# Kernel tuning notes

Measured on AMD Instinct MI355X. Metric: run time of the kernel, lower is better.

Reference implementation:

```python
import jax, jax.numpy as jnp
import numpy as np

# MANO kinematic tree (21-joint ordering: wrist=0, fingers 1..15, tips 16..20)
PARENTS16 = [0, 0, 1, 2, 0, 4, 5, 0, 7, 8, 0, 10, 11, 0, 13, 14]
MANOIDX = [2, 3, 17, 5, 6, 18, 8, 9, 20, 11, 12, 19, 14, 15, 16]
MANOPDX = [1, 2, 3, 4, 5, 6, 7, 8, 9, 10, 11, 12, 13, 14, 15]
CHILDREN = [[1, 2, 3, 17, 4, 5, 6, 18, 7, 8, 9, 20, 10, 11, 12, 19, 13, 14, 15, 16],
            [2, 3, 17], [3, 17], [17], [5, 6, 18], [6, 18], [18],
            [8, 9, 20], [9, 20], [20], [11, 12, 19], [12, 19], [19],
            [14, 15, 16], [15, 16], [16]]
TIPS = [(17, 3), (18, 6), (20, 9), (19, 12), (16, 15)]
EPS = 1e-8


def _skew(v):
    # v: (N,3) -> (N,3,3) skew-symmetric cross-product matrix
    z = jnp.zeros_like(v[..., 0])
    return jnp.stack([
        jnp.stack([z, -v[..., 2], v[..., 1]], -1),
        jnp.stack([v[..., 2], z, -v[..., 0]], -1),
        jnp.stack([-v[..., 1], v[..., 0], z], -1)], -2)


def _rot_between(v0, v1):
    # Rodrigues rotation taking direction v0 to v1. (N,3),(N,3) -> (N,3,3)
    n0 = v0 / (jnp.linalg.norm(v0, axis=-1, keepdims=True) + EPS)
    n1 = v1 / (jnp.linalg.norm(v1, axis=-1, keepdims=True) + EPS)
    c = jnp.sum(n0 * n1, axis=-1)
    ax = jnp.cross(n0, n1)
    s = jnp.linalg.norm(ax, axis=-1)
    axn = ax / (s[..., None] + EPS)
    K = _skew(axn)
    I = jnp.eye(3, dtype=v0.dtype)
    return I + s[:, None, None] * K + (1.0 - c)[:, None, None] * (K @ K)


def _kabsch(a, b):
    # rotation R (N,3,3) minimizing ||R a_i - b_i|| over joints; a,b: (N,21,3)
    H = jnp.einsum('nji,njk->nik', a, b)
    U, S, Vt = jnp.linalg.svd(H)
    V = jnp.swapaxes(Vt, -1, -2)
    d = jnp.linalg.det(V @ jnp.swapaxes(U, -1, -2))
    scale = jnp.stack([jnp.ones_like(d), jnp.ones_like(d), d], axis=-1)  # (N,3)
    Vd = V * scale[:, None, :]
    return Vd @ jnp.swapaxes(U, -1, -2)


def setup_inputs() -> dict:
    key = jax.random.key(0)
    k1, k2 = jax.random.split(key)
    N = 400000
    joint_gt = jax.random.normal(k1, (N, 21, 3), dtype=jnp.float32)
    tempJ = jax.random.normal(k2, (N, 21, 3), dtype=jnp.float32)
    return {"joint_gt": joint_gt, "tempJ": tempJ}


def _kinematic_match(joint_gt, tempJ):
    oriWrist = joint_gt[:, :1]
    jg = joint_gt - oriWrist                  # GT joints, wrist-centered
    tJ0 = tempJ - tempJ[:, :1]                # template (tempJori), wrist-centered
    tJ = tJ0

    # global wrist rotation aligning template to GT (wristRotTorch)
    Rw = _kabsch(tJ, jg)
    tJ = jnp.einsum('nij,ncj->nci', Rw, tJ)   # apply to all joints (wrist stays 0)

    Grot = [None] * 16
    locals_rot = [None] * 16
    Grot[0] = Rw

    # greedy per-joint rotation fitting with parent->child propagation
    for idx, i in enumerate(MANOIDX):
        pi = MANOPDX[idx]
        v0 = tJ[:, i] - tJ[:, pi]
        v1 = jg[:, i] - tJ[:, pi]
        r = _rot_between(v0, v1)              # (N,3,3)
        t0 = tJ[:, pi]
        ch = CHILDREN[pi]
        rel = tJ[:, ch] - t0[:, None]
        tJ = tJ.at[:, ch].set(jnp.einsum('nij,ncj->nci', r, rel) + t0[:, None])
        p16 = PARENTS16[idx + 1]
        GpR = Grot[p16]
        Grot[idx + 1] = r @ GpR               # transformG = L @ Gp (rotation part)
        # transformLmano = inv(Gp) @ L @ Gp  (rotation part)
        locals_rot[idx + 1] = jnp.einsum('nji,njk,nkl->nil', GpR, r, GpR)

    # rotate2joint: forward kinematics from mano-local rotations over template
    Gfk = [None] * 16
    Gfk[0] = Rw
    pos = jnp.zeros_like(jg)
    for k in range(1, 16):
        p = PARENTS16[k]
        off = tJ0[:, k] - tJ0[:, p]
        pos = pos.at[:, k].set(jnp.einsum('nij,nj->ni', Gfk[p], off) + pos[:, p])
        Gfk[k] = Gfk[p] @ locals_rot[k]
    for tip, par in TIPS:
        off = tJ0[:, tip] - tJ0[:, par]
        pos = pos.at[:, tip].set(jnp.einsum('nij,nj->ni', Gfk[par], off) + pos[:, par])

    return pos + oriWrist


def reference(joint_gt, tempJ):
    return _kinematic_match(joint_gt, tempJ)
```

## Files before the change

### kernel.cpp

```cpp
#include <hip/hip_runtime.h>

#define DEVI __device__ __forceinline__

static constexpr float KEPS = 1e-8f;

DEVI float frcp(float x) { return __builtin_amdgcn_rcpf(x); }
DEVI float frsq(float x) { return __builtin_amdgcn_rsqf(x); }

template<int P, int Q>
DEVI void jrot(float A[4][4], float V[4][4]) {
  float apq = A[P][Q];
  if (fabsf(apq) > 1e-20f) {
    float theta = (A[Q][Q] - A[P][P]) * 0.5f * frcp(apq);
    float t = copysignf(frcp(fabsf(theta) + sqrtf(theta * theta + 1.0f)), theta);
    float c = frsq(t * t + 1.0f);
    float s = t * c;
#pragma unroll
    for (int k = 0; k < 4; ++k) { float u = A[k][P], v = A[k][Q]; A[k][P] = c*u - s*v; A[k][Q] = s*u + c*v; }
#pragma unroll
    for (int k = 0; k < 4; ++k) { float u = A[P][k], v = A[Q][k]; A[P][k] = c*u - s*v; A[Q][k] = s*u + c*v; }
#pragma unroll
    for (int k = 0; k < 4; ++k) { float u = V[k][P], v = V[k][Q]; V[k][P] = c*u - s*v; V[k][Q] = s*u + c*v; }
  }
}

template<int C>
DEVI void rotc(float t[21][3], float px, float py, float pz,
               float r00, float r01, float r02,
               float r10, float r11, float r12,
               float r20, float r21, float r22) {
  float x = t[C][0] - px, y = t[C][1] - py, z = t[C][2] - pz;
  t[C][0] = r00*x + r01*y + r02*z + px;
  t[C][1] = r10*x + r11*y + r12*z + py;
  t[C][2] = r20*x + r21*y + r22*z + pz;
}

template<int PI, int I, int C0, int C1, int C2, int NC>
DEVI void bone(float t[21][3], const float g[21][3]) {
  float px = t[PI][0], py = t[PI][1], pz = t[PI][2];
  float v0x = t[I][0] - px, v0y = t[I][1] - py, v0z = t[I][2] - pz;
  float v1x = g[I][0] - px, v1y = g[I][1] - py, v1z = g[I][2] - pz;
  float in0 = frcp(sqrtf(v0x*v0x + v0y*v0y + v0z*v0z) + KEPS);
  float in1 = frcp(sqrtf(v1x*v1x + v1y*v1y + v1z*v1z) + KEPS);
  float ax = v0x*in0, ay = v0y*in0, az = v0z*in0;
  float bx = v1x*in1, by = v1y*in1, bz = v1z*in1;
  float c = ax*bx + ay*by + az*bz;
  float cx = ay*bz - az*by;
  float cy = az*bx - ax*bz;
  float cz = ax*by - ay*bx;
  float s = sqrtf(cx*cx + cy*cy + cz*cz);
  float is = frcp(s + KEPS);
  float kx = cx*is, ky = cy*is, kz = cz*is;
  float omc = 1.0f - c;
  float r00 = 1.0f - omc*(ky*ky + kz*kz);
  float r11 = 1.0f - omc*(kx*kx + kz*kz);
  float r22 = 1.0f - omc*(kx*kx + ky*ky);
  float kxy = omc*kx*ky, kxz = omc*kx*kz, kyz = omc*ky*kz;
  float skx = s*kx, sky = s*ky, skz = s*kz;
  float r01 = kxy - skz, r10 = kxy + skz;
  float r02 = kxz + sky, r20 = kxz - sky;
  float r12 = kyz - skx, r21 = kyz + skx;
  rotc<C0>(t, px, py, pz, r00, r01, r02, r10, r11, r12, r20, r21, r22);
  if constexpr (NC > 1) rotc<C1>(t, px, py, pz, r00, r01, r02, r10, r11, r12, r20, r21, r22);
  if constexpr (NC > 2) rotc<C2>(t, px, py, pz, r00, r01, r02, r10, r11, r12, r20, r21, r22);
}

template<int B, int T>
DEVI void finger(float t[21][3], const float g[21][3]) {
  bone<B,     B + 1, B + 1, B + 2, T, 3>(t, g);
  bone<B + 1, B + 2, B + 2, T,     T, 2>(t, g);
  bone<B + 2, T,     T,     T,     T, 1>(t, g);
}

DEVI void stage_half(float* lds, const float* __restrict__ src, long long off,
                     long long total, bool fullblk, int tid) {
  if (fullblk) {
    const float4* s4 = (const float4*)(src + off);
#pragma unroll
    for (int it = 0; it < 8; ++it) { int i = it * 64 + tid; if (i < 504) ((float4*)lds)[i] = s4[i]; }
  } else {
    for (int i = tid; i < 2016; i += 64) { long long gi = off + i; lds[i] = (gi < total) ? src[gi] : 0.0f; }
  }
}

__global__ void __launch_bounds__(64)
kin_kernel(const float* __restrict__ joint_gt, const float* __restrict__ tempJ,
           float* __restrict__ out, int N) {
  __shared__ float lds[32 * 63];
  const int tid = threadIdx.x;
  const int half = tid >> 5;
  const int lane = tid & 31;
  const long long base = (long long)blockIdx.x * (64LL * 63);
  const long long total = (long long)N * 63;
  const bool fullblk = (base + 64LL * 63) <= total;

  float t[21][3], g[21][3];
  float wx, wy, wz;

#pragma unroll 1
  for (int h = 0; h < 2; ++h) {
    stage_half(lds, tempJ, base + (long long)h * 2016, total, fullblk, tid);
    __syncthreads();
    if (half == h) {
      const float* p = lds + lane * 63;
      float rx = p[0], ry = p[1], rz = p[2];
#pragma unroll
      for (int j = 0; j < 21; ++j) {
        t[j][0] = p[3 * j + 0] - rx;
        t[j][1] = p[3 * j + 1] - ry;
        t[j][2] = p[3 * j + 2] - rz;
      }
    }
    __syncthreads();
  }

#pragma unroll 1
  for (int h = 0; h < 2; ++h) {
    stage_half(lds, joint_gt, base + (long long)h * 2016, total, fullblk, tid);
    __syncthreads();
    if (half == h) {
      const float* p = lds + lane * 63;
      wx = p[0]; wy = p[1]; wz = p[2];
#pragma unroll
      for (int j = 0; j < 21; ++j) {
        g[j][0] = p[3 * j + 0] - wx;
        g[j][1] = p[3 * j + 1] - wy;
        g[j][2] = p[3 * j + 2] - wz;
      }
    }
    __syncthreads();
  }

  float H[3][3] = {{0, 0, 0}, {0, 0, 0}, {0, 0, 0}};
#pragma unroll
  for (int j = 0; j < 21; ++j)
#pragma unroll
    for (int a = 0; a < 3; ++a)
#pragma unroll
      for (int b = 0; b < 3; ++b)
        H[a][b] += t[j][a] * g[j][b];

  float Sxx = H[0][0], Sxy = H[0][1], Sxz = H[0][2];
  float Syx = H[1][0], Syy = H[1][1], Syz = H[1][2];
  float Szx = H[2][0], Szy = H[2][1], Szz = H[2][2];
  float A[4][4] = {
    {  Sxx + Syy + Szz, Syz - Szy,        Szx - Sxz,        Sxy - Syx },
    {  Syz - Szy,       Sxx - Syy - Szz,  Sxy + Syx,        Szx + Sxz },
    {  Szx - Sxz,       Sxy + Syx,       -Sxx + Syy - Szz,  Syz + Szy },
    {  Sxy - Syx,       Szx + Sxz,        Syz + Szy,       -Sxx - Syy + Szz }};
  float V[4][4] = {{1,0,0,0},{0,1,0,0},{0,0,1,0},{0,0,0,1}};
#pragma unroll 1
  for (int sw = 0; sw < 6; ++sw) {
    jrot<0,1>(A, V); jrot<0,2>(A, V); jrot<0,3>(A, V);
    jrot<1,2>(A, V); jrot<1,3>(A, V); jrot<2,3>(A, V);
  }
  float e  = A[0][0];
  float qw = V[0][0], qx = V[1][0], qy = V[2][0], qz = V[3][0];
#define PICK(K) { bool bb = A[K][K] > e; e = bb ? A[K][K] : e; \
  qw = bb ? V[0][K] : qw; qx = bb ? V[1][K] : qx; qy = bb ? V[2][K] : qy; qz = bb ? V[3][K] : qz; }
  PICK(1) PICK(2) PICK(3)
#undef PICK
  float qn = frsq(qw*qw + qx*qx + qy*qy + qz*qz);
  qw *= qn; qx *= qn; qy *= qn; qz *= qn;
  float R00 = 1.0f - 2.0f*(qy*qy + qz*qz), R01 = 2.0f*(qx*qy - qw*qz), R02 = 2.0f*(qx*qz + qw*qy);
  float R10 = 2.0f*(qx*qy + qw*qz), R11 = 1.0f - 2.0f*(qx*qx + qz*qz), R12 = 2.0f*(qy*qz - qw*qx);
  float R20 = 2.0f*(qx*qz - qw*qy), R21 = 2.0f*(qy*qz + qw*qx), R22 = 1.0f - 2.0f*(qx*qx + qy*qy);

#pragma unroll
  for (int j = 1; j < 21; ++j) {
    float x = t[j][0], y = t[j][1], z = t[j][2];
    t[j][0] = R00*x + R01*y + R02*z;
    t[j][1] = R10*x + R11*y + R12*z;
    t[j][2] = R20*x + R21*y + R22*z;
  }

  finger<1, 17>(t, g);
  finger<4, 18>(t, g);
  finger<7, 20>(t, g);
  finger<10, 19>(t, g);
  finger<13, 16>(t, g);

#pragma unroll 1
  for (int h = 0; h < 2; ++h) {
    if (half == h) {
      float* p = lds + lane * 63;
#pragma unroll
      for (int j = 0; j < 21; ++j) {
        p[3 * j + 0] = t[j][0] + wx;
        p[3 * j + 1] = t[j][1] + wy;
        p[3 * j + 2] = t[j][2] + wz;
      }
    }
    __syncthreads();
    const long long off = base + (long long)h * 2016;
    if (fullblk) {
      float4* d4 = (float4*)(out + off);
#pragma unroll
      for (int it = 0; it < 8; ++it) { int i = it * 64 + tid; if (i < 504) d4[i] = ((const float4*)lds)[i]; }
    } else {
      for (int i = tid; i < 2016; i += 64) { long long gi = off + i; if (gi < total) out[gi] = lds[i]; }
    }
    __syncthreads();
  }
}

extern "C" void kernel_launch(void* const* d_in, const int* in_sizes, int n_in,
                              void* d_out, int out_size, void* d_ws, size_t ws_size,
                              hipStream_t stream) {
  const float* joint_gt = (const float*)d_in[0];
  const float* tempJ    = (const float*)d_in[1];
  float* out = (float*)d_out;
  int N = in_sizes[0] / 63;
  int blocks = (N + 63) / 64;
  hipLaunchKernelGGL(kin_kernel, dim3(blocks), dim3(64), 0, stream,
                     joint_gt, tempJ, out, N);
}
```

Measured before the change: 325.7 us.

## Use per-wave LDS staging without block barriers and pack four waves per block

Each wave now owns its own LDS slice and stages inputs and outputs in four 16-item rounds, so all __syncthreads calls are removed and the code relies on wave-level lockstep. Blocks grow from 64 to 256 threads with launch bounds (256,4), and the LDS per wave shrinks. The aim is to cut barrier stalls and raise occupancy for this register-heavy kernel. In exchange there are more, smaller staging rounds, and correctness depends on implicit wave synchronization through LDS.

```diff
diff --git a/kernel.cpp b/kernel.cpp
--- a/kernel.cpp
+++ b/kernel.cpp
@@ -72,37 +72,33 @@
   bone<B + 2, T,     T,     T,     T, 1>(t, g);
 }
 
-DEVI void stage_half(float* lds, const float* __restrict__ src, long long off,
-                     long long total, bool fullblk, int tid) {
-  if (fullblk) {
-    const float4* s4 = (const float4*)(src + off);
-#pragma unroll
-    for (int it = 0; it < 8; ++it) { int i = it * 64 + tid; if (i < 504) ((float4*)lds)[i] = s4[i]; }
-  } else {
-    for (int i = tid; i < 2016; i += 64) { long long gi = off + i; lds[i] = (gi < total) ? src[gi] : 0.0f; }
-  }
-}
-
-__global__ void __launch_bounds__(64)
+__global__ void __launch_bounds__(256, 4)
 kin_kernel(const float* __restrict__ joint_gt, const float* __restrict__ tempJ,
            float* __restrict__ out, int N) {
-  __shared__ float lds[32 * 63];
-  const int tid = threadIdx.x;
-  const int half = tid >> 5;
-  const int lane = tid & 31;
-  const long long base = (long long)blockIdx.x * (64LL * 63);
+  __shared__ float lds[4][16 * 63];
+  const int wave = threadIdx.x >> 6;
+  const int lane = threadIdx.x & 63;
+  float* buf = &lds[wave][0];
+  const long long item0 = ((long long)blockIdx.x * 4 + wave) * 64;
+  if (item0 >= N) return;
+  const bool wfull = (item0 + 64) <= (long long)N;
   const long long total = (long long)N * 63;
-  const bool fullblk = (base + 64LL * 63) <= total;
 
   float t[21][3], g[21][3];
   float wx, wy, wz;
 
 #pragma unroll 1
-  for (int h = 0; h < 2; ++h) {
-    stage_half(lds, tempJ, base + (long long)h * 2016, total, fullblk, tid);
-    __syncthreads();
-    if (half == h) {
-      const float* p = lds + lane * 63;
+  for (int r = 0; r < 4; ++r) {
+    const long long off = (item0 + r * 16) * 63;
+    if (wfull) {
+      const float4* s4 = (const float4*)(tempJ + off);
+#pragma unroll
+      for (int k = 0; k < 4; ++k) { int i = k * 64 + lane; if (i < 252) ((float4*)buf)[i] = s4[i]; }
+    } else {
+      for (int i = lane; i < 1008; i += 64) { long long gi = off + i; buf[i] = (gi < total) ? tempJ[gi] : 0.0f; }
+    }
+    if ((lane >> 4) == r) {
+      const float* p = buf + (lane & 15) * 63;
       float rx = p[0], ry = p[1], rz = p[2];
 #pragma unroll
       for (int j = 0; j < 21; ++j) {
@@ -111,15 +107,20 @@
         t[j][2] = p[3 * j + 2] - rz;
       }
     }
-    __syncthreads();
-  }
-
-#pragma unroll 1
-  for (int h = 0; h < 2; ++h) {
-    stage_half(lds, joint_gt, base + (long long)h * 2016, total, fullblk, tid);
-    __syncthreads();
-    if (half == h) {
-      const float* p = lds + lane * 63;
+  }
+
+#pragma unroll 1
+  for (int r = 0; r < 4; ++r) {
+    const long long off = (item0 + r * 16) * 63;
+    if (wfull) {
+      const float4* s4 = (const float4*)(joint_gt + off);
+#pragma unroll
+      for (int k = 0; k < 4; ++k) { int i = k * 64 + lane; if (i < 252) ((float4*)buf)[i] = s4[i]; }
+    } else {
+      for (int i = lane; i < 1008; i += 64) { long long gi = off + i; buf[i] = (gi < total) ? joint_gt[gi] : 0.0f; }
+    }
+    if ((lane >> 4) == r) {
+      const float* p = buf + (lane & 15) * 63;
       wx = p[0]; wy = p[1]; wz = p[2];
 #pragma unroll
       for (int j = 0; j < 21; ++j) {
@@ -128,7 +129,6 @@
         g[j][2] = p[3 * j + 2] - wz;
       }
     }
-    __syncthreads();
   }
 
   float H[3][3] = {{0, 0, 0}, {0, 0, 0}, {0, 0, 0}};
@@ -181,9 +181,9 @@
   finger<13, 16>(t, g);
 
 #pragma unroll 1
-  for (int h = 0; h < 2; ++h) {
-    if (half == h) {
-      float* p = lds + lane * 63;
+  for (int r = 0; r < 4; ++r) {
+    if ((lane >> 4) == r) {
+      float* p = buf + (lane & 15) * 63;
 #pragma unroll
       for (int j = 0; j < 21; ++j) {
         p[3 * j + 0] = t[j][0] + wx;
@@ -191,16 +191,14 @@
         p[3 * j + 2] = t[j][2] + wz;
       }
     }
-    __syncthreads();
-    const long long off = base + (long long)h * 2016;
-    if (fullblk) {
+    const long long off = (item0 + r * 16) * 63;
+    if (wfull) {
       float4* d4 = (float4*)(out + off);
 #pragma unroll
-      for (int it = 0; it < 8; ++it) { int i = it * 64 + tid; if (i < 504) d4[i] = ((const float4*)lds)[i]; }
+      for (int k = 0; k < 4; ++k) { int i = k * 64 + lane; if (i < 252) d4[i] = ((const float4*)buf)[i]; }
     } else {
-      for (int i = tid; i < 2016; i += 64) { long long gi = off + i; if (gi < total) out[gi] = lds[i]; }
-    }
-    __syncthreads();
+      for (int i = lane; i < 1008; i += 64) { long long gi = off + i; if (gi < total) out[gi] = buf[i]; }
+    }
   }
 }
 
@@ -211,7 +209,8 @@
   const float* tempJ    = (const float*)d_in[1];
   float* out = (float*)d_out;
   int N = in_sizes[0] / 63;
-  int blocks = (N + 63) / 64;
-  hipLaunchKernelGGL(kin_kernel, dim3(blocks), dim3(64), 0, stream,
+  int waves = (N + 63) / 64;
+  int blocks = (waves + 3) / 4;
+  hipLaunchKernelGGL(kin_kernel, dim3(blocks), dim3(256), 0, stream,
                      joint_gt, tempJ, out, N);
 }
```

Result: slower. 380.8 us (+16.9%).
